# Optimization experiments

Measured on AMD Instinct MI355X. Metric: run time of the kernel, lower is better.

Reference implementation:

```python
import jax, jax.numpy as jnp
import numpy as np

MARGIN = 0.2
EPS = 1e-6  # F.pairwise_distance default eps (added to the difference)


def _cdist(x):
    # Euclidean pairwise distances, [N, N]
    sq = jnp.sum(x * x, axis=1)
    d2 = sq[:, None] + sq[None, :] - 2.0 * (x @ x.T)
    return jnp.sqrt(jnp.maximum(d2, 0.0))


def setup_inputs() -> dict:
    key = jax.random.key(0)
    k1, k2 = jax.random.split(key)
    features = jax.random.normal(k1, (8192, 128), dtype=jnp.float32)
    labels = jax.random.randint(k2, (8192,), 0, 512)
    return {"features": features, "labels": labels}


def reference(features, labels):
    # Distances are used only for (non-differentiable) index selection.
    dists = jax.lax.stop_gradient(_cdist(features))
    pos_mask = labels[None, :] == labels[:, None]  # includes diagonal (self), as in the torch loop
    neg_mask = ~pos_mask

    # Batch-hard mining, vectorized over all anchor rows:
    # hardest positive = max dist among same-label; hardest negative = min dist among different-label.
    pos_idx = jnp.argmax(jnp.where(pos_mask, dists, -jnp.inf), axis=1)
    neg_idx = jnp.argmin(jnp.where(neg_mask, dists, jnp.inf), axis=1)
    # Anchor is skipped in the original loop only if it has no negatives.
    valid = jnp.any(neg_mask, axis=1)

    anchors = features
    pos = features[pos_idx]
    neg = features[neg_idx]

    # F.pairwise_distance(x1, x2, p=2) == ||x1 - x2 + eps||_2
    pos_d = jnp.linalg.norm(anchors - pos + EPS, axis=1)
    neg_d = jnp.linalg.norm(anchors - neg + EPS, axis=1)
    per_anchor = jax.nn.relu(pos_d - neg_d + MARGIN)

    cnt = jnp.sum(valid)
    loss = jnp.where(
        cnt > 0,
        jnp.sum(jnp.where(valid, per_anchor, 0.0)) / jnp.maximum(cnt, 1).astype(per_anchor.dtype),
        jnp.zeros((), per_anchor.dtype),
    )
    return loss
```

## Files before the change

### kernel.cpp

```cpp
#include <hip/hip_runtime.h>
#include <hip/hip_bf16.h>

#define N 8192
#define DIMS 128
#define NSLICE 32
#define SLICE_COLS (N / NSLICE)
#define SUBTILES (SLICE_COLS / 16)
#define NSTEPS (SUBTILES / 2)
#define ROWS_PER_BLOCK 256
#define STRIPS 4
#define NROWBLK (N / ROWS_PER_BLOCK)
#define NFIN 2048
#define MARGIN_F 0.2f
#define EPS_F 1e-6f
#define BIAS_F 512.0f
#define INF_F __builtin_huge_valf()

typedef __bf16 bf16x8 __attribute__((ext_vector_type(8)));
typedef float f32x4 __attribute__((ext_vector_type(4)));

#define XB_OFF   0
#define META_OFF 2097152
#define PART_OFF 2162688
#define BSUM_OFF 4259840

#define GLD_LDS(g, l) \
  __builtin_amdgcn_global_load_lds( \
      (const __attribute__((address_space(1))) void*)(g), \
      (__attribute__((address_space(3))) void*)(l), 16, 0, 0)

__global__ __launch_bounds__(256) void prep_kernel(
    const float* __restrict__ feat, const int* __restrict__ lab,
    unsigned short* __restrict__ Xb, float2* __restrict__ meta) {
  int row = blockIdx.x * 4 + (threadIdx.x >> 6);
  int lane = threadIdx.x & 63;
  float2 x = *reinterpret_cast<const float2*>(feat + (size_t)row * DIMS + lane * 2);
  __hip_bfloat16 hx = __float2bfloat16(x.x);
  __hip_bfloat16 hy = __float2bfloat16(x.y);
  unsigned short ux, uy;
  __builtin_memcpy(&ux, &hx, 2);
  __builtin_memcpy(&uy, &hy, 2);
  unsigned int packed = (unsigned int)ux | ((unsigned int)uy << 16);
  *reinterpret_cast<unsigned int*>(Xb + (size_t)row * DIMS + lane * 2) = packed;
  float s = x.x * x.x + x.y * x.y;
#pragma unroll
  for (int m = 32; m >= 1; m >>= 1) s += __shfl_xor(s, m, 64);
  if (lane == 0) meta[row] = make_float2(s + BIAS_F, __int_as_float(lab[row]));
}

__global__ __launch_bounds__(256, 3) void mine_kernel(
    const unsigned short* __restrict__ Xb, const float2* __restrict__ meta,
    const int* __restrict__ lab, uint2* __restrict__ part) {
  __shared__ char smem[2 * 8192 + 2048];

  int rb = blockIdx.x / NSLICE;
  int sl = blockIdx.x % NSLICE;
  int tid = threadIdx.x;
  int wave = tid >> 6;
  int lane = tid & 63;
  int lrow = lane & 15;
  int lk = lane >> 4;
  int rowbase = rb * ROWS_PER_BLOCK + wave * (STRIPS * 16);
  int j0 = sl * SLICE_COLS;

  if (wave < 2) {
    const char* g = (const char*)meta + (size_t)j0 * 8 + tid * 16;
    char* l = smem + 16384 + wave * 1024;
    GLD_LDS(g, l);
  }
  int colt = tid >> 4;
  int chunk = tid & 15;
  const char* gsrc0 = (const char*)Xb + (size_t)(j0 + colt) * 256 +
                      ((chunk ^ (colt & 7)) * 16);
  {
    GLD_LDS(gsrc0, smem + wave * 1024);
    GLD_LDS(gsrc0 + 4096, smem + 4096 + wave * 1024);
  }

  bf16x8 afrag[STRIPS][4];
#pragma unroll
  for (int s = 0; s < STRIPS; ++s) {
    const unsigned short* rp = Xb + (size_t)(rowbase + s * 16 + lrow) * DIMS;
#pragma unroll
    for (int g = 0; g < 4; ++g)
      afrag[s][g] = *reinterpret_cast<const bf16x8*>(rp + g * 32 + lk * 8);
  }
  int4 labi[STRIPS];
#pragma unroll
  for (int s = 0; s < STRIPS; ++s)
    labi[s] = *reinterpret_cast<const int4*>(lab + rowbase + s * 16 + lk * 4);

  unsigned int bpu[STRIPS][4], bnu[STRIPS][4];
#pragma unroll
  for (int s = 0; s < STRIPS; ++s)
#pragma unroll
    for (int e = 0; e < 4; ++e) { bpu[s][e] = 0u; bnu[s][e] = 0xFFFFFFFFu; }

  int boff[4];
#pragma unroll
  for (int g = 0; g < 4; ++g)
    boff[g] = lrow * 256 + (((g * 4 + lk) ^ (lrow & 7)) * 16);

  __syncthreads();

  for (int it = 0; it < NSTEPS; ++it) {
    int cur = it & 1;
    if (it + 1 < NSTEPS) {
      const char* g = gsrc0 + (size_t)(it + 1) * 8192;
      char* l = smem + (cur ^ 1) * 8192 + wave * 1024;
      GLD_LDS(g, l);
      GLD_LDS(g + 4096, l + 4096);
    }

#pragma unroll
    for (int h = 0; h < 2; ++h) {
      int t = it * 2 + h;
      float2 mcur =
          *reinterpret_cast<const float2*>(smem + 16384 + t * 128 + lrow * 8);
      float sqjB = mcur.x;
      int labj = __float_as_int(mcur.y);
      unsigned int ju = (unsigned int)(j0 + t * 16 + lrow);

      const char* bbase = smem + cur * 8192 + h * 4096;
      bf16x8 bb[4];
#pragma unroll
      for (int g = 0; g < 4; ++g)
        bb[g] = *reinterpret_cast<const bf16x8*>(bbase + boff[g]);

#pragma unroll
      for (int s = 0; s < STRIPS; ++s) {
        f32x4 acc = {0.f, 0.f, 0.f, 0.f};
#pragma unroll
        for (int g = 0; g < 4; ++g)
          acc = __builtin_amdgcn_mfma_f32_16x16x32_bf16(afrag[s][g], bb[g], acc,
                                                        0, 0, 0);
        int labs[4] = {labi[s].x, labi[s].y, labi[s].z, labi[s].w};
#pragma unroll
        for (int e = 0; e < 4; ++e) {
          float key = fmaf(-2.0f, acc[e], sqjB);
          unsigned int u = (__float_as_uint(key) & 0xFFFFE000u) | ju;
          bool pos = (labj == labs[e]);
          unsigned int up = pos ? u : 0u;
          unsigned int un = pos ? 0xFFFFFFFFu : u;
          bpu[s][e] = max(bpu[s][e], up);
          bnu[s][e] = min(bnu[s][e], un);
        }
      }
    }
    __syncthreads();
  }

#pragma unroll
  for (int s = 0; s < STRIPS; ++s) {
#pragma unroll
    for (int e = 0; e < 4; ++e) {
      unsigned int pu = bpu[s][e], nu = bnu[s][e];
#pragma unroll
      for (int m = 1; m < 16; m <<= 1) {
        pu = max(pu, (unsigned int)__shfl_xor((int)pu, m, 64));
        nu = min(nu, (unsigned int)__shfl_xor((int)nu, m, 64));
      }
      if (lrow == 0) {
        int row = rowbase + s * 16 + lk * 4 + e;
        part[(size_t)sl * N + row] = make_uint2(pu, nu);
      }
    }
  }
}

__global__ __launch_bounds__(256) void finalize_kernel(
    const float* __restrict__ feat, const uint2* __restrict__ part,
    float2* __restrict__ bsum) {
  int wave = threadIdx.x >> 6, lane = threadIdx.x & 63;
  int i = blockIdx.x * 4 + wave;

  unsigned int pu = 0u, nu = 0xFFFFFFFFu;
  if (lane < NSLICE) {
    uint2 p = part[(size_t)lane * N + i];
    pu = p.x; nu = p.y;
  }
#pragma unroll
  for (int m = 1; m < 32; m <<= 1) {
    pu = max(pu, (unsigned int)__shfl_xor((int)pu, m, 64));
    nu = min(nu, (unsigned int)__shfl_xor((int)nu, m, 64));
  }
  pu = (unsigned int)__shfl((int)pu, 0, 64);
  nu = (unsigned int)__shfl((int)nu, 0, 64);
  bool valid = (nu != 0xFFFFFFFFu);
  int pi = (int)(pu & 8191u);
  int ni = (int)(nu & 8191u);

  float2 av = *reinterpret_cast<const float2*>(feat + (size_t)i * DIMS + lane * 2);
  float2 pw = *reinterpret_cast<const float2*>(feat + (size_t)pi * DIMS + lane * 2);
  float2 nw = *reinterpret_cast<const float2*>(feat + (size_t)ni * DIMS + lane * 2);
  float d0 = av.x - pw.x + EPS_F, d1 = av.y - pw.y + EPS_F;
  float sp = fmaf(d0, d0, d1 * d1);
  float e0 = av.x - nw.x + EPS_F, e1 = av.y - nw.y + EPS_F;
  float sn = fmaf(e0, e0, e1 * e1);
#pragma unroll
  for (int m = 32; m >= 1; m >>= 1) {
    sp += __shfl_xor(sp, m, 64);
    sn += __shfl_xor(sn, m, 64);
  }

  __shared__ float s_s[4], s_c[4];
  if (lane == 0) {
    float per = sqrtf(sp) - sqrtf(sn) + MARGIN_F;
    per = per > 0.f ? per : 0.f;
    per = valid ? per : 0.f;
    s_s[wave] = per;
    s_c[wave] = valid ? 1.f : 0.f;
  }
  __syncthreads();
  if (threadIdx.x == 0) {
    float ts = (s_s[0] + s_s[1]) + (s_s[2] + s_s[3]);
    float tc = (s_c[0] + s_c[1]) + (s_c[2] + s_c[3]);
    bsum[blockIdx.x] = make_float2(ts, tc);
  }
}

__global__ __launch_bounds__(256) void final_reduce_kernel(
    const float2* __restrict__ bsum, float* __restrict__ out) {
  int t = threadIdx.x;
  float s = 0.f, c = 0.f;
#pragma unroll
  for (int k = 0; k < NFIN / 256; ++k) {
    float2 v = bsum[t + k * 256];
    s += v.x; c += v.y;
  }
#pragma unroll
  for (int m = 32; m >= 1; m >>= 1) {
    s += __shfl_xor(s, m, 64);
    c += __shfl_xor(c, m, 64);
  }
  __shared__ float s_s[4], s_c[4];
  int wave = t >> 6, lane = t & 63;
  if (lane == 0) { s_s[wave] = s; s_c[wave] = c; }
  __syncthreads();
  if (t == 0) {
    float ts = (s_s[0] + s_s[1]) + (s_s[2] + s_s[3]);
    float tc = (s_c[0] + s_c[1]) + (s_c[2] + s_c[3]);
    out[0] = (tc > 0.f) ? (ts / tc) : 0.f;
  }
}

extern "C" void kernel_launch(void* const* d_in, const int* in_sizes, int n_in,
                              void* d_out, int out_size, void* d_ws, size_t ws_size,
                              hipStream_t stream) {
  const float* feat = (const float*)d_in[0];
  const int* lab = (const int*)d_in[1];
  char* ws = (char*)d_ws;
  unsigned short* Xb = (unsigned short*)(ws + XB_OFF);
  float2* meta = (float2*)(ws + META_OFF);
  uint2* part = (uint2*)(ws + PART_OFF);
  float2* bsum = (float2*)(ws + BSUM_OFF);
  float* out = (float*)d_out;

  prep_kernel<<<N / 4, 256, 0, stream>>>(feat, lab, Xb, meta);
  mine_kernel<<<NROWBLK * NSLICE, 256, 0, stream>>>(Xb, meta, lab, part);
  finalize_kernel<<<N / 4, 256, 0, stream>>>(feat, part, bsum);
  final_reduce_kernel<<<1, 256, 0, stream>>>(bsum, out);
}
```

Measured before the change: 47.71 us.

## Deepen B-tile LDS pipeline to four buffers with explicit vmcnt waits

The mining kernel's double-buffered B-tile staging becomes a 4-slot ring buffer with three tiles prefetched ahead. The loop is fully unrolled, and each step uses an explicit s_waitcnt vmcnt plus a single barrier in place of the per-iteration __syncthreads. This is meant to hide global-to-LDS load latency and cut the wait per step. LDS use per block roughly doubles (about 34KB), which could limit occupancy, though 3 blocks per CU still fits.

```diff
diff --git a/kernel.cpp b/kernel.cpp
--- a/kernel.cpp
+++ b/kernel.cpp
@@ -14,6 +14,7 @@
 #define MARGIN_F 0.2f
 #define EPS_F 1e-6f
 #define BIAS_F 512.0f
+#define META_LDS 32768
 #define INF_F __builtin_huge_valf()
 
 typedef __bf16 bf16x8 __attribute__((ext_vector_type(8)));
@@ -51,7 +52,7 @@
 __global__ __launch_bounds__(256, 3) void mine_kernel(
     const unsigned short* __restrict__ Xb, const float2* __restrict__ meta,
     const int* __restrict__ lab, uint2* __restrict__ part) {
-  __shared__ char smem[2 * 8192 + 2048];
+  __shared__ char smem[4 * 8192 + 2048];
 
   int rb = blockIdx.x / NSLICE;
   int sl = blockIdx.x % NSLICE;
@@ -65,16 +66,19 @@
 
   if (wave < 2) {
     const char* g = (const char*)meta + (size_t)j0 * 8 + tid * 16;
-    char* l = smem + 16384 + wave * 1024;
+    char* l = smem + META_LDS + wave * 1024;
     GLD_LDS(g, l);
   }
   int colt = tid >> 4;
   int chunk = tid & 15;
   const char* gsrc0 = (const char*)Xb + (size_t)(j0 + colt) * 256 +
                       ((chunk ^ (colt & 7)) * 16);
-  {
-    GLD_LDS(gsrc0, smem + wave * 1024);
-    GLD_LDS(gsrc0 + 4096, smem + 4096 + wave * 1024);
+#pragma unroll
+  for (int s = 0; s < 3; ++s) {
+    const char* g = gsrc0 + (size_t)s * 8192;
+    char* l = smem + s * 8192 + wave * 1024;
+    GLD_LDS(g, l);
+    GLD_LDS(g + 4096, l + 4096);
   }
 
   bf16x8 afrag[STRIPS][4];
@@ -103,52 +107,61 @@
 
   __syncthreads();
 
-  for (int it = 0; it < NSTEPS; ++it) {
-    int cur = it & 1;
-    if (it + 1 < NSTEPS) {
-      const char* g = gsrc0 + (size_t)(it + 1) * 8192;
-      char* l = smem + (cur ^ 1) * 8192 + wave * 1024;
-      GLD_LDS(g, l);
-      GLD_LDS(g + 4096, l + 4096);
-    }
-
-#pragma unroll
-    for (int h = 0; h < 2; ++h) {
-      int t = it * 2 + h;
-      float2 mcur =
-          *reinterpret_cast<const float2*>(smem + 16384 + t * 128 + lrow * 8);
-      float sqjB = mcur.x;
-      int labj = __float_as_int(mcur.y);
-      unsigned int ju = (unsigned int)(j0 + t * 16 + lrow);
-
-      const char* bbase = smem + cur * 8192 + h * 4096;
-      bf16x8 bb[4];
-#pragma unroll
-      for (int g = 0; g < 4; ++g)
-        bb[g] = *reinterpret_cast<const bf16x8*>(bbase + boff[g]);
-
-#pragma unroll
-      for (int s = 0; s < STRIPS; ++s) {
-        f32x4 acc = {0.f, 0.f, 0.f, 0.f};
-#pragma unroll
-        for (int g = 0; g < 4; ++g)
-          acc = __builtin_amdgcn_mfma_f32_16x16x32_bf16(afrag[s][g], bb[g], acc,
-                                                        0, 0, 0);
-        int labs[4] = {labi[s].x, labi[s].y, labi[s].z, labi[s].w};
-#pragma unroll
-        for (int e = 0; e < 4; ++e) {
-          float key = fmaf(-2.0f, acc[e], sqjB);
-          unsigned int u = (__float_as_uint(key) & 0xFFFFE000u) | ju;
-          bool pos = (labj == labs[e]);
-          unsigned int up = pos ? u : 0u;
-          unsigned int un = pos ? 0xFFFFFFFFu : u;
-          bpu[s][e] = max(bpu[s][e], up);
-          bnu[s][e] = min(bnu[s][e], un);
-        }
-      }
-    }
-    __syncthreads();
-  }
+#define COMPUTE_SUBTILE(BUFOFS, T)                                           \
+  {                                                                          \
+    float2 mcur = *reinterpret_cast<const float2*>(                          \
+        smem + META_LDS + (T) * 128 + lrow * 8);                             \
+    float sqjB = mcur.x;                                                     \
+    int labj = __float_as_int(mcur.y);                                       \
+    unsigned int ju = (unsigned int)(j0 + (T) * 16 + lrow);                  \
+    const char* bbase = smem + (BUFOFS);                                     \
+    bf16x8 bb[4];                                                            \
+    _Pragma("unroll") for (int g = 0; g < 4; ++g)                            \
+        bb[g] = *reinterpret_cast<const bf16x8*>(bbase + boff[g]);           \
+    _Pragma("unroll") for (int s = 0; s < STRIPS; ++s) {                     \
+      f32x4 acc = {0.f, 0.f, 0.f, 0.f};                                      \
+      _Pragma("unroll") for (int g = 0; g < 4; ++g)                          \
+          acc = __builtin_amdgcn_mfma_f32_16x16x32_bf16(afrag[s][g], bb[g],  \
+                                                        acc, 0, 0, 0);       \
+      int labs[4] = {labi[s].x, labi[s].y, labi[s].z, labi[s].w};            \
+      _Pragma("unroll") for (int e = 0; e < 4; ++e) {                        \
+        float key = fmaf(-2.0f, acc[e], sqjB);                               \
+        unsigned int u = (__float_as_uint(key) & 0xFFFFE000u) | ju;          \
+        bool pos = (labj == labs[e]);                                        \
+        unsigned int up = pos ? u : 0u;                                      \
+        unsigned int un = pos ? 0xFFFFFFFFu : u;                             \
+        bpu[s][e] = max(bpu[s][e], up);                                      \
+        bnu[s][e] = min(bnu[s][e], un);                                      \
+      }                                                                      \
+    }                                                                        \
+  }
+
+#define DO_STEP(IT, NW)                                                      \
+  {                                                                          \
+    asm volatile("s_waitcnt vmcnt(" #NW ")" ::: "memory");                   \
+    __builtin_amdgcn_s_barrier();                                            \
+    __builtin_amdgcn_sched_barrier(0);                                       \
+    if ((IT) + 3 < NSTEPS) {                                                 \
+      const char* g = gsrc0 + (size_t)((IT) + 3) * 8192;                     \
+      char* l = smem + (((IT) + 3) & 3) * 8192 + wave * 1024;                \
+      GLD_LDS(g, l);                                                         \
+      GLD_LDS(g + 4096, l + 4096);                                           \
+    }                                                                        \
+    COMPUTE_SUBTILE(((IT) & 3) * 8192, 2 * (IT));                            \
+    COMPUTE_SUBTILE(((IT) & 3) * 8192 + 4096, 2 * (IT) + 1);                 \
+  }
+
+  DO_STEP(0, 4)
+  DO_STEP(1, 4)
+  DO_STEP(2, 4)
+  DO_STEP(3, 4)
+  DO_STEP(4, 4)
+  DO_STEP(5, 4)
+  DO_STEP(6, 2)
+  DO_STEP(7, 0)
+
+#undef DO_STEP
+#undef COMPUTE_SUBTILE
 
 #pragma unroll
   for (int s = 0; s < STRIPS; ++s) {
```

After: 181.3 us. 280% more time.
